# Performance work log

Measured on AMD Instinct MI355X. Metric: run time of the kernel, lower is better.

## Reference

```python
import jax, jax.numpy as jnp
import numpy as np

B, C, L = 16, 128, 2048


def setup_inputs() -> dict:
    key = jax.random.key(0)
    ks = jax.random.split(key, 7)
    s = 1.0 / np.sqrt(C)  # torch Conv1d default init scale
    x = jax.random.normal(ks[0], (B, C, L), dtype=jnp.float32)
    W1 = jax.random.uniform(ks[1], (C, C), jnp.float32, -s, s)
    b1 = jax.random.uniform(ks[2], (C,), jnp.float32, -s, s)
    W2 = jax.random.uniform(ks[3], (C, C), jnp.float32, -s, s)
    b2 = jax.random.uniform(ks[4], (C,), jnp.float32, -s, s)
    W3 = jax.random.uniform(ks[5], (C, C), jnp.float32, -s, s)
    b3 = jax.random.uniform(ks[6], (C,), jnp.float32, -s, s)
    return {"x": x, "W1": W1, "b1": b1, "W2": W2, "b2": b2, "W3": W3, "b3": b3}


def _conv1x1(x, W, b):
    # x: [B,C,L], W: [out,in] -> [B,out,L]
    return jnp.einsum('oc,bcl->bol', W, x) + b[None, :, None]


def reference(x, W1, b1, W2, b2, W3, b3):
    q = _conv1x1(x, W1, b1).transpose(0, 2, 1)  # [B,L,C]
    k = _conv1x1(x, W2, b2).transpose(0, 2, 1)  # [B,L,C]
    v = _conv1x1(x, W3, b3).transpose(0, 2, 1)  # [B,L,C]
    attn = jnp.einsum('bic,bjc->bij', q, k)     # [B,L,L]
    attn = jax.nn.softmax(attn, axis=-1)
    out = jnp.einsum('bij,bjc->bic', attn, v)   # [B,L,C]
    return out.transpose(0, 2, 1)               # [B,C,L]
```

## Files before the change

### kernel.cpp

```cpp
#include <hip/hip_runtime.h>
#include <hip/hip_bf16.h>
#include <stdint.h>

#define B_ 16
#define C_ 128
#define L_ 2048
#define LOG2E 1.4426950408889634f

typedef __attribute__((ext_vector_type(8))) short bf16x8;
typedef __attribute__((ext_vector_type(4))) float f32x4;
typedef __attribute__((ext_vector_type(16))) float f32x16;
typedef __attribute__((ext_vector_type(4))) unsigned int u32x4;

typedef __attribute__((address_space(3))) unsigned int lds_u32_t;
typedef const __attribute__((address_space(1))) unsigned int gbl_u32_t;

__device__ __forceinline__ void gload_lds16(const void* g, void* l) {
  __builtin_amdgcn_global_load_lds((gbl_u32_t*)g,
                                   (lds_u32_t*)(unsigned long long)l, 16, 0, 0);
}

__device__ __forceinline__ unsigned short f2bf(float x) {
  union { float f; unsigned u; } v; v.f = x;
  unsigned u = v.u;
  u += 0x7fffu + ((u >> 16) & 1u);
  return (unsigned short)(u >> 16);
}

__device__ __forceinline__ unsigned pk2(float a, float b) {
  return (unsigned)f2bf(a) | ((unsigned)f2bf(b) << 16);
}

__device__ __forceinline__ unsigned cvtpk_bf16(float lo, float hi_) {
  unsigned r;
  asm("v_cvt_pk_bf16_f32 %0, %1, %2" : "=v"(r) : "v"(lo), "v"(hi_));
  return r;
}

__device__ __forceinline__ f32x16 z16() {
  f32x16 v;
#pragma unroll
  for (int i = 0; i < 16; ++i) v[i] = 0.f;
  return v;
}

__device__ __forceinline__ float tmax16(const f32x16& v) {
  float a0 = fmaxf(v[0], v[1]),  a1 = fmaxf(v[2], v[3]);
  float a2 = fmaxf(v[4], v[5]),  a3 = fmaxf(v[6], v[7]);
  float a4 = fmaxf(v[8], v[9]),  a5 = fmaxf(v[10], v[11]);
  float a6 = fmaxf(v[12], v[13]), a7 = fmaxf(v[14], v[15]);
  float b0 = fmaxf(a0, a1), b1 = fmaxf(a2, a3);
  float b2 = fmaxf(a4, a5), b3 = fmaxf(a6, a7);
  return fmaxf(fmaxf(b0, b1), fmaxf(b2, b3));
}

__device__ __forceinline__ float tsum16(const f32x16& v) {
  float a0 = v[0] + v[1],  a1 = v[2] + v[3];
  float a2 = v[4] + v[5],  a3 = v[6] + v[7];
  float a4 = v[8] + v[9],  a5 = v[10] + v[11];
  float a6 = v[12] + v[13], a7 = v[14] + v[15];
  float b0 = a0 + a1, b1 = a2 + a3, b2 = a4 + a5, b3 = a6 + a7;
  return (b0 + b1) + (b2 + b3);
}

__global__ __launch_bounds__(256, 2) void proj_kernel(
    const float* __restrict__ x,
    const float* __restrict__ W1, const float* __restrict__ b1,
    const float* __restrict__ W2, const float* __restrict__ b2,
    const float* __restrict__ W3, const float* __restrict__ b3,
    unsigned short* __restrict__ Qo, unsigned short* __restrict__ Ko,
    unsigned short* __restrict__ Vt)
{
  __shared__ unsigned short Xt[64][136];
  __shared__ unsigned short Wl[128][136];

  const int b  = blockIdx.x & 15;
  const int lt = blockIdx.x >> 4;
  const int l0 = lt * 64;
  const int tid = threadIdx.x;
  const int w = tid >> 6, lane = tid & 63, li = lane & 15, lg = lane >> 4;

  for (int it = 0; it < 8; ++it) {
    int idx = tid + it * 256;
    int c = idx >> 4, f4 = idx & 15;
    const float4 vv = *(const float4*)(x + (size_t)(b * C_ + c) * L_ + l0 + f4 * 4);
    Xt[f4 * 4 + 0][c] = f2bf(vv.x);
    Xt[f4 * 4 + 1][c] = f2bf(vv.y);
    Xt[f4 * 4 + 2][c] = f2bf(vv.z);
    Xt[f4 * 4 + 3][c] = f2bf(vv.w);
  }

  auto stageW = [&](const float* W) {
    for (int it = 0; it < 16; ++it) {
      int idx = tid + it * 256;
      int o = idx >> 5, f4 = idx & 31;
      const float4 vv = *(const float4*)(W + (size_t)o * C_ + f4 * 4);
      unsigned short* p = &Wl[o][f4 * 4];
      p[0] = f2bf(vv.x); p[1] = f2bf(vv.y); p[2] = f2bf(vv.z); p[3] = f2bf(vv.w);
    }
  };

  auto computePhase = [&](const float* bias, unsigned short* Out, int mode, float sc) {
    f32x4 acc[8];
#pragma unroll
    for (int ni = 0; ni < 8; ++ni) acc[ni] = (f32x4){0.f, 0.f, 0.f, 0.f};
    bf16x8 af[4];
#pragma unroll
    for (int kk = 0; kk < 4; ++kk)
      af[kk] = *(const bf16x8*)&Xt[w * 16 + li][lg * 8 + kk * 32];
#pragma unroll
    for (int kk = 0; kk < 4; ++kk) {
#pragma unroll
      for (int ni = 0; ni < 8; ++ni) {
        bf16x8 bf = *(const bf16x8*)&Wl[ni * 16 + li][lg * 8 + kk * 32];
        acc[ni] = __builtin_amdgcn_mfma_f32_16x16x32_bf16(af[kk], bf, acc[ni], 0, 0, 0);
      }
    }
    if (mode == 0) {
#pragma unroll
      for (int ni = 0; ni < 8; ++ni) {
        float bv = bias[ni * 16 + li];
#pragma unroll
        for (int r = 0; r < 4; ++r) {
          int lrow = l0 + w * 16 + lg * 4 + r;
          Out[(size_t)(b * L_ + lrow) * C_ + ni * 16 + li] = f2bf((acc[ni][r] + bv) * sc);
        }
      }
    } else {
#pragma unroll
      for (int ni = 0; ni < 8; ++ni) {
        float bv = bias[ni * 16 + li];
        int o = ni * 16 + li;
        unsigned long long pw =
            (unsigned long long)pk2(acc[ni][0] + bv, acc[ni][1] + bv) |
            ((unsigned long long)pk2(acc[ni][2] + bv, acc[ni][3] + bv) << 32);
        *(unsigned long long*)(Out + (size_t)(b * C_ + o) * L_ + l0 + w * 16 + lg * 4) = pw;
      }
    }
  };

  stageW(W1);
  __syncthreads();
  computePhase(b1, Qo, 0, LOG2E);
  __syncthreads();
  stageW(W2);
  __syncthreads();
  computePhase(b2, Ko, 0, 1.0f);
  __syncthreads();
  stageW(W3);
  __syncthreads();
  computePhase(b3, Vt, 1, 1.0f);
}

__global__ __launch_bounds__(512, 2) void attn_kernel(
    const unsigned short* __restrict__ Q,
    const unsigned short* __restrict__ K,
    const unsigned short* __restrict__ Vt,
    float* __restrict__ out)
{
  __shared__ char smem[65536 + 2048];

  const int b  = blockIdx.x & 15;
  const int qt = blockIdx.x >> 4;
  const int tid = threadIdx.x;
  const int w = tid >> 6, lane = tid & 63;
  const int q32 = lane & 31, hi = lane >> 5;
  const int qg = w >> 1, jh = w & 1;
  const int qrow = qt * 128 + qg * 32 + q32;
  const size_t bLC = (size_t)b * L_ * C_;

  bf16x8 qf[8];
  {
    const unsigned short* qp = Q + bLC + (size_t)qrow * C_ + hi * 8;
#pragma unroll
    for (int kt = 0; kt < 8; ++kt) qf[kt] = *(const bf16x8*)(qp + kt * 16);
  }

  f32x16 oacc[4];
#pragma unroll
  for (int i = 0; i < 4; ++i) oacc[i] = z16();
  float m2 = -3e38f, lrun = 0.f;

  const char* kgb = (const char*)(K + bLC);
  const char* vgb = (const char*)(Vt + bLC);

  auto stage = [&](int sel, int t) {
    if (w < 4) {
      const char* ktb = kgb + (size_t)t * (64 * 256);
      char* dst = smem + sel * 16384 + (w & 3) * 4096;
#pragma unroll
      for (int i2 = 0; i2 < 4; ++i2) {
        int d = (w & 3) * 4096 + i2 * 1024 + lane * 16;
        int row = d >> 8, cb = d & 255;
        gload_lds16(ktb + row * 256 + (cb ^ ((row & 15) << 4)), dst + i2 * 1024);
      }
    } else {
      const char* vt0 = vgb + (size_t)t * 128;
      char* dst = smem + 32768 + sel * 16384 + (w & 3) * 4096;
#pragma unroll
      for (int i2 = 0; i2 < 4; ++i2) {
        int d = (w & 3) * 4096 + i2 * 1024 + lane * 16;
        int rc = d >> 7, cv = d & 127;
        gload_lds16(vt0 + (size_t)rc * (L_ * 2) + (cv ^ ((rc & 7) << 4)), dst + i2 * 1024);
      }
    }
  };

  stage(0, 0);
  __syncthreads();

  int cur = 0;
  for (int t = 0; t < 32; ++t) {
    if (t + 1 < 32) stage(cur ^ 1, t + 1);

    const char* kb = smem + cur * 16384;
    const int krow = jh * 32 + q32;
    const int kro  = krow << 8, ksw = (krow & 15) << 4;
    f32x16 sA = z16(), sB = z16();
    __builtin_amdgcn_s_setprio(1);
#pragma unroll
    for (int kt2 = 0; kt2 < 4; ++kt2) {
      bf16x8 kf0 = *(const bf16x8*)(kb + kro + ((kt2 * 32 + hi * 16) ^ ksw));
      bf16x8 kf1 = *(const bf16x8*)(kb + kro + (((kt2 + 4) * 32 + hi * 16) ^ ksw));
      sA = __builtin_amdgcn_mfma_f32_32x32x16_bf16(kf0, qf[kt2], sA, 0, 0, 0);
      sB = __builtin_amdgcn_mfma_f32_32x32x16_bf16(kf1, qf[kt2 + 4], sB, 0, 0, 0);
    }
    __builtin_amdgcn_s_setprio(0);
    f32x16 s;
#pragma unroll
    for (int r = 0; r < 16; ++r) s[r] = sA[r] + sB[r];

    float pm = tmax16(s);
    pm = fmaxf(pm, __shfl_xor(pm, 32));
    if (!__all(pm - m2 <= 8.f)) {
      float mn = fmaxf(m2, pm);
      float al = exp2f(m2 - mn);
      lrun *= al;
#pragma unroll
      for (int ct = 0; ct < 4; ++ct) oacc[ct] = oacc[ct] * al;
      m2 = mn;
    }
#pragma unroll
    for (int r = 0; r < 16; ++r) s[r] = exp2f(s[r] - m2);
    float ps = tsum16(s);
    ps += __shfl_xor(ps, 32);
    lrun += ps;

    bf16x8 pf[2];
#pragma unroll
    for (int kj = 0; kj < 2; ++kj) {
      const int base = kj * 8;
      unsigned wl0 = cvtpk_bf16(s[base + 0], s[base + 1]);
      unsigned wl1 = cvtpk_bf16(s[base + 2], s[base + 3]);
      unsigned wh0 = cvtpk_bf16(s[base + 4], s[base + 5]);
      unsigned wh1 = cvtpk_bf16(s[base + 6], s[base + 7]);
      unsigned snd0 = hi ? wl0 : wh0;
      unsigned snd1 = hi ? wl1 : wh1;
      unsigned rcv0 = (unsigned)__shfl_xor((int)snd0, 32);
      unsigned rcv1 = (unsigned)__shfl_xor((int)snd1, 32);
      unsigned w0 = hi ? rcv0 : wl0;
      unsigned w1 = hi ? rcv1 : wl1;
      unsigned w2 = hi ? wh0 : rcv0;
      unsigned w3 = hi ? wh1 : rcv1;
      u32x4 pw = {w0, w1, w2, w3};
      pf[kj] = *reinterpret_cast<bf16x8*>(&pw);
    }

    const char* vb = smem + 32768 + cur * 16384;
    __builtin_amdgcn_s_setprio(1);
#pragma unroll
    for (int kj = 0; kj < 2; ++kj) {
      const int kjg = jh * 2 + kj;
#pragma unroll
      for (int ct = 0; ct < 4; ++ct) {
        int rowc = ct * 32 + q32;
        bf16x8 vf = *(const bf16x8*)(vb + (rowc << 7) +
                                     ((kjg * 32 + hi * 16) ^ ((rowc & 7) << 4)));
        oacc[ct] = __builtin_amdgcn_mfma_f32_32x32x16_bf16(vf, pf[kj], oacc[ct], 0, 0, 0);
      }
    }
    __builtin_amdgcn_s_setprio(0);

    __syncthreads();
    cur ^= 1;
  }

  float* mlb = (float*)(smem + 65536);
  if (hi == 0) {
    mlb[(w * 32 + q32) * 2 + 0] = m2;
    mlb[(w * 32 + q32) * 2 + 1] = lrun;
  }
  __syncthreads();
  const float mB = mlb[((w ^ 1) * 32 + q32) * 2 + 0];
  const float lB = mlb[((w ^ 1) * 32 + q32) * 2 + 1];
  const float mstar = fmaxf(m2, mB);
  const float aown  = exp2f(m2 - mstar);
  float* scrb = (float*)smem + (size_t)(qg * 64 + lane) * 33;
  float* ob = out + (size_t)b * C_ * L_ + qrow;
  float inv = 0.f;
  if (jh == 0) {
    const float aB = exp2f(mB - mstar);
    inv = 1.0f / (lrun * aown + lB * aB);
  }
  __syncthreads();
  if (jh == 1) {
#pragma unroll
    for (int r = 0; r < 16; ++r) {
      scrb[r]      = oacc[0][r] * aown;
      scrb[16 + r] = oacc[1][r] * aown;
    }
  }
  __syncthreads();
  if (jh == 0) {
#pragma unroll
    for (int ct = 0; ct < 2; ++ct)
#pragma unroll
      for (int r = 0; r < 16; ++r) {
        float v = oacc[ct][r] * aown + scrb[ct * 16 + r];
        int c = ct * 32 + (r & 3) + 8 * (r >> 2) + 4 * hi;
        ob[(size_t)c * L_] = v * inv;
      }
  }
  __syncthreads();
  if (jh == 1) {
#pragma unroll
    for (int r = 0; r < 16; ++r) {
      scrb[r]      = oacc[2][r] * aown;
      scrb[16 + r] = oacc[3][r] * aown;
    }
  }
  __syncthreads();
  if (jh == 0) {
#pragma unroll
    for (int ct = 0; ct < 2; ++ct)
#pragma unroll
      for (int r = 0; r < 16; ++r) {
        float v = oacc[2 + ct][r] * aown + scrb[ct * 16 + r];
        int c = (2 + ct) * 32 + (r & 3) + 8 * (r >> 2) + 4 * hi;
        ob[(size_t)c * L_] = v * inv;
      }
  }
}

extern "C" void kernel_launch(void* const* d_in, const int* in_sizes, int n_in,
                              void* d_out, int out_size, void* d_ws, size_t ws_size,
                              hipStream_t stream) {
  (void)in_sizes; (void)n_in; (void)out_size; (void)ws_size;
  const float* x  = (const float*)d_in[0];
  const float* W1 = (const float*)d_in[1];
  const float* b1 = (const float*)d_in[2];
  const float* W2 = (const float*)d_in[3];
  const float* b2 = (const float*)d_in[4];
  const float* W3 = (const float*)d_in[5];
  const float* b3 = (const float*)d_in[6];

  unsigned short* Q  = (unsigned short*)d_ws;
  unsigned short* K  = Q + (size_t)B_ * L_ * C_;
  unsigned short* Vt = K + (size_t)B_ * L_ * C_;

  proj_kernel<<<512, 256, 0, stream>>>(x, W1, b1, W2, b2, W3, b3, Q, K, Vt);
  attn_kernel<<<256, 512, 0, stream>>>(Q, K, Vt, (float*)d_out);
}
```

Baseline: 74.72 us.

## Halve attention block to 64 query rows, use single MFMA chain and max3

```diff
diff --git a/kernel.cpp b/kernel.cpp
--- a/kernel.cpp
+++ b/kernel.cpp
@@ -37,6 +37,12 @@
   return r;
 }
 
+__device__ __forceinline__ float max3f(float a, float b, float c) {
+  float r;
+  asm("v_max3_f32 %0, %1, %2, %3" : "=v"(r) : "v"(a), "v"(b), "v"(c));
+  return r;
+}
+
 __device__ __forceinline__ f32x16 z16() {
   f32x16 v;
 #pragma unroll
@@ -45,13 +51,14 @@
 }
 
 __device__ __forceinline__ float tmax16(const f32x16& v) {
-  float a0 = fmaxf(v[0], v[1]),  a1 = fmaxf(v[2], v[3]);
-  float a2 = fmaxf(v[4], v[5]),  a3 = fmaxf(v[6], v[7]);
-  float a4 = fmaxf(v[8], v[9]),  a5 = fmaxf(v[10], v[11]);
-  float a6 = fmaxf(v[12], v[13]), a7 = fmaxf(v[14], v[15]);
-  float b0 = fmaxf(a0, a1), b1 = fmaxf(a2, a3);
-  float b2 = fmaxf(a4, a5), b3 = fmaxf(a6, a7);
-  return fmaxf(fmaxf(b0, b1), fmaxf(b2, b3));
+  float m0 = max3f(v[0], v[1], v[2]);
+  float m1 = max3f(v[3], v[4], v[5]);
+  float m2_ = max3f(v[6], v[7], v[8]);
+  float m3 = max3f(v[9], v[10], v[11]);
+  float m4 = max3f(v[12], v[13], v[14]);
+  float a = max3f(m0, m1, m2_);
+  float b = max3f(m3, m4, v[15]);
+  return fmaxf(a, b);
 }
 
 __device__ __forceinline__ float tsum16(const f32x16& v) {
@@ -152,21 +159,21 @@
   computePhase(b3, Vt, 1, 1.0f);
 }
 
-__global__ __launch_bounds__(512, 2) void attn_kernel(
+__global__ __launch_bounds__(256, 2) void attn_kernel(
     const unsigned short* __restrict__ Q,
     const unsigned short* __restrict__ K,
     const unsigned short* __restrict__ Vt,
     float* __restrict__ out)
 {
-  __shared__ char smem[65536 + 2048];
+  __shared__ char smem[65536 + 1024];
 
   const int b  = blockIdx.x & 15;
   const int qt = blockIdx.x >> 4;
   const int tid = threadIdx.x;
   const int w = tid >> 6, lane = tid & 63;
   const int q32 = lane & 31, hi = lane >> 5;
-  const int qg = w >> 1, jh = w & 1;
-  const int qrow = qt * 128 + qg * 32 + q32;
+  const int qg = (w >> 1) & 1, jh = w & 1;
+  const int qrow = qt * 64 + qg * 32 + q32;
   const size_t bLC = (size_t)b * L_ * C_;
 
   bf16x8 qf[8];
@@ -185,21 +192,21 @@
   const char* vgb = (const char*)(Vt + bLC);
 
   auto stage = [&](int sel, int t) {
-    if (w < 4) {
+    if (w < 2) {
       const char* ktb = kgb + (size_t)t * (64 * 256);
-      char* dst = smem + sel * 16384 + (w & 3) * 4096;
-#pragma unroll
-      for (int i2 = 0; i2 < 4; ++i2) {
-        int d = (w & 3) * 4096 + i2 * 1024 + lane * 16;
+      char* dst = smem + sel * 16384 + w * 8192;
+#pragma unroll
+      for (int i2 = 0; i2 < 8; ++i2) {
+        int d = w * 8192 + i2 * 1024 + lane * 16;
         int row = d >> 8, cb = d & 255;
         gload_lds16(ktb + row * 256 + (cb ^ ((row & 15) << 4)), dst + i2 * 1024);
       }
     } else {
       const char* vt0 = vgb + (size_t)t * 128;
-      char* dst = smem + 32768 + sel * 16384 + (w & 3) * 4096;
-#pragma unroll
-      for (int i2 = 0; i2 < 4; ++i2) {
-        int d = (w & 3) * 4096 + i2 * 1024 + lane * 16;
+      char* dst = smem + 32768 + sel * 16384 + (w - 2) * 8192;
+#pragma unroll
+      for (int i2 = 0; i2 < 8; ++i2) {
+        int d = (w - 2) * 8192 + i2 * 1024 + lane * 16;
         int rc = d >> 7, cv = d & 127;
         gload_lds16(vt0 + (size_t)rc * (L_ * 2) + (cv ^ ((rc & 7) << 4)), dst + i2 * 1024);
       }
@@ -216,19 +223,14 @@
     const char* kb = smem + cur * 16384;
     const int krow = jh * 32 + q32;
     const int kro  = krow << 8, ksw = (krow & 15) << 4;
-    f32x16 sA = z16(), sB = z16();
+    f32x16 s = z16();
     __builtin_amdgcn_s_setprio(1);
 #pragma unroll
-    for (int kt2 = 0; kt2 < 4; ++kt2) {
-      bf16x8 kf0 = *(const bf16x8*)(kb + kro + ((kt2 * 32 + hi * 16) ^ ksw));
-      bf16x8 kf1 = *(const bf16x8*)(kb + kro + (((kt2 + 4) * 32 + hi * 16) ^ ksw));
-      sA = __builtin_amdgcn_mfma_f32_32x32x16_bf16(kf0, qf[kt2], sA, 0, 0, 0);
-      sB = __builtin_amdgcn_mfma_f32_32x32x16_bf16(kf1, qf[kt2 + 4], sB, 0, 0, 0);
+    for (int kt2 = 0; kt2 < 8; ++kt2) {
+      bf16x8 kf = *(const bf16x8*)(kb + kro + ((kt2 * 32 + hi * 16) ^ ksw));
+      s = __builtin_amdgcn_mfma_f32_32x32x16_bf16(kf, qf[kt2], s, 0, 0, 0);
     }
     __builtin_amdgcn_s_setprio(0);
-    f32x16 s;
-#pragma unroll
-    for (int r = 0; r < 16; ++r) s[r] = sA[r] + sB[r];
 
     float pm = tmax16(s);
     pm = fmaxf(pm, __shfl_xor(pm, 32));
@@ -359,5 +361,5 @@
   unsigned short* Vt = K + (size_t)B_ * L_ * C_;
 
   proj_kernel<<<512, 256, 0, stream>>>(x, W1, b1, W2, b2, W3, b3, Q, K, Vt);
-  attn_kernel<<<256, 512, 0, stream>>>(Q, K, Vt, (float*)d_out);
-}
+  attn_kernel<<<512, 256, 0, stream>>>(Q, K, Vt, (float*)d_out);
+}
```

Measured after the change: 77.74 us. +4.0%, slower.
